# Kernel optimization log

Measured on AMD Instinct MI355X. Metric: run time of the kernel, lower is better.

## Reference

```python
import jax, jax.numpy as jnp
import numpy as np

NUM_CLASSES = 10
NPTS = 100            # quadrature points per unit interval (torch default npts=100)
EPS = 1e-5            # self.epsilon in the torch module
BATCH = 131072
C_IN = 512


def _betaln(a, b):
    return jax.lax.lgamma(a) + jax.lax.lgamma(b) - jax.lax.lgamma(a + b)


def setup_inputs() -> dict:
    key = jax.random.key(0)
    k1, k2, k3, k4, k5 = jax.random.split(key, 5)
    s = 1.0 / np.sqrt(C_IN).astype(np.float32)
    x = jax.random.normal(k1, (BATCH, C_IN), dtype=jnp.float32)
    W_alpha = jax.random.normal(k2, (C_IN, 1), dtype=jnp.float32) * s
    b_alpha = jax.random.normal(k3, (1,), dtype=jnp.float32) * s
    W_beta = jax.random.normal(k4, (C_IN, 1), dtype=jnp.float32) * s
    b_beta = jax.random.normal(k5, (1,), dtype=jnp.float32) * s
    return {"x": x, "W_alpha": W_alpha, "b_alpha": b_alpha,
            "W_beta": W_beta, "b_beta": b_beta}


def reference(x, W_alpha, b_alpha, W_beta, b_beta):
    # alpha, beta: [B, 1], clamp(1 + softplus(linear(x)), 1, 100)
    alpha = jnp.clip(1.0 + jax.nn.softplus(x @ W_alpha + b_alpha), 1.0, 100.0)
    beta = jnp.clip(1.0 + jax.nn.softplus(x @ W_beta + b_beta), 1.0, 100.0)
    lbeta = _betaln(alpha, beta)  # [B, 1] log Beta-function normalizer
    dx = 1.0 / (NPTS * NUM_CLASSES)

    def unnorm_cdf(b_thr):
        # torch: linspace(eps, b-eps, int(npts*b)); Beta.log_prob broadcast [B, n]
        n = int(NPTS * b_thr)
        if n == 0:
            return jnp.zeros((x.shape[0],), dtype=x.dtype)
        grid = jnp.linspace(EPS, b_thr - EPS, n, dtype=x.dtype)  # [n]
        logpdf = ((alpha - 1.0) * jnp.log(grid)
                  + (beta - 1.0) * jnp.log1p(-grid)
                  - lbeta)  # [B, n]
        return jnp.exp(logpdf).sum(axis=1) * dx  # [B]

    # thresholds i/C for i = 0..C (static Python loop over C+1 small fixed set)
    cdfs = [unnorm_cdf(i / NUM_CLASSES) for i in range(NUM_CLASSES + 1)]
    probs = jnp.stack([cdfs[i + 1] - cdfs[i] for i in range(NUM_CLASSES)], axis=1)  # [B, C]
    # torch uses diag(1/rowsum) @ probs == row-broadcast normalization
    return probs / probs.sum(axis=1, keepdims=True)
```

## Files before the change

kernel.cpp:

```cpp
#include <hip/hip_runtime.h>
#include <math.h>

#define EPS_F 1e-5f
#define NPOINTS 550
#define CIN 512

static __device__ __forceinline__ float softplus_f(float z) {
    return fmaxf(z, 0.0f) + log1pf(expf(-fabsf(z)));
}

static __device__ __forceinline__ float dot8(const float4 a0, const float4 a1,
                                             const float4 w0, const float4 w1) {
    float s = a0.x * w0.x;
    s = fmaf(a0.y, w0.y, s);
    s = fmaf(a0.z, w0.z, s);
    s = fmaf(a0.w, w0.w, s);
    s = fmaf(a1.x, w1.x, s);
    s = fmaf(a1.y, w1.y, s);
    s = fmaf(a1.z, w1.z, s);
    s = fmaf(a1.w, w1.w, s);
    return s;
}

__global__ __launch_bounds__(256, 8) void beta_unimodal_kernel(
    const float* __restrict__ x,
    const float* __restrict__ Wa, const float* __restrict__ ba,
    const float* __restrict__ Wb, const float* __restrict__ bb,
    float* __restrict__ out)
{
    __shared__ float2 tab[NPOINTS];
    __shared__ float outbuf[64 * 10];

    const int tid = threadIdx.x;

    for (int p = tid; p < NPOINTS; p += 256) {
        int i = 1, off = 0;
        while (p >= off + 10 * i) { off += 10 * i; ++i; }
        const int j = p - off;
        const int n = 10 * i;
        const float thr = (float)i * 0.1f;
        const float step = (thr - 2.0f * EPS_F) / (float)(n - 1);
        const float g = EPS_F + step * (float)j;
        float2 e;
        e.x = log2f(g);
        e.y = log2f(1.0f - g);
        tab[p] = e;
    }
    __syncthreads();

    const int lane = tid & 63;
    const int wave = tid >> 6;
    const long rowBase = (long)blockIdx.x * 64 + wave * 16;

    const float4* Wa4 = (const float4*)Wa;
    const float4* Wb4 = (const float4*)Wb;
    const float4 wa0 = Wa4[lane], wa1 = Wa4[64 + lane];
    const float4 wb0 = Wb4[lane], wb1 = Wb4[64 + lane];

    const int g = lane >> 2;
    const int q = lane & 3;
    float my_da = 0.0f, my_db = 0.0f;

    for (int r0 = 0; r0 < 16; r0 += 4) {
        float4 xs0[4], xs1[4];
        #pragma unroll
        for (int u = 0; u < 4; ++u) {
            const float4* xr = (const float4*)(x + (rowBase + r0 + u) * CIN);
            xs0[u] = xr[lane];
            xs1[u] = xr[64 + lane];
        }
        #pragma unroll
        for (int u = 0; u < 4; ++u) {
            float da = dot8(xs0[u], xs1[u], wa0, wa1);
            float db = dot8(xs0[u], xs1[u], wb0, wb1);
            #pragma unroll
            for (int s = 32; s > 0; s >>= 1) {
                da += __shfl_xor(da, s, 64);
                db += __shfl_xor(db, s, 64);
            }
            if (g == r0 + u) { my_da = da; my_db = db; }
        }
    }

    const float za = my_da + ba[0];
    const float zb = my_db + bb[0];
    const float alpha = fminf(fmaxf(1.0f + softplus_f(za), 1.0f), 100.0f);
    const float beta  = fminf(fmaxf(1.0f + softplus_f(zb), 1.0f), 100.0f);
    const float am1 = alpha - 1.0f;
    const float bm1 = beta - 1.0f;

    const float denom = am1 + bm1;
    float mode = (denom > 0.0f) ? (am1 / denom) : 0.5f;
    mode = fminf(fmaxf(mode, 1e-7f), 1.0f - 1.1920929e-7f);
    const float M2 = am1 * log2f(mode) + bm1 * log2f(1.0f - mode);

    float seg[10];
    int p0 = 0;
    #pragma unroll
    for (int i = 1; i <= 10; ++i) {
        const int n = 10 * i;
        float s = 0.0f;
        for (int j = q; j < n; j += 4) {
            const float2 t = tab[p0 + j];
            const float e = fmaf(am1, t.x, bm1 * t.y) - M2;
            s += __builtin_amdgcn_exp2f(e);
        }
        s += __shfl_xor(s, 1, 64);
        s += __shfl_xor(s, 2, 64);
        seg[i - 1] = s;
        p0 += n;
    }

    const float inv = 1.0f / seg[9];
    const int rowLocal = wave * 16 + g;
    for (int k = q; k < 10; k += 4) {
        const float prev = (k > 0) ? seg[k - 1] : 0.0f;
        outbuf[rowLocal * 10 + k] = (seg[k] - prev) * inv;
    }
    __syncthreads();

    if (tid < 160) {
        const float4* src = (const float4*)outbuf;
        float4* dst = (float4*)(out + (size_t)blockIdx.x * 640);
        dst[tid] = src[tid];
    }
}

extern "C" void kernel_launch(void* const* d_in, const int* in_sizes, int n_in,
                              void* d_out, int out_size, void* d_ws, size_t ws_size,
                              hipStream_t stream) {
    const float* x  = (const float*)d_in[0];
    const float* Wa = (const float*)d_in[1];
    const float* ba = (const float*)d_in[2];
    const float* Wb = (const float*)d_in[3];
    const float* bb = (const float*)d_in[4];
    float* out = (float*)d_out;

    const int batch = in_sizes[0] / CIN;
    const int blocks = batch / 64;
    beta_unimodal_kernel<<<blocks, 256, 0, stream>>>(x, Wa, ba, Wb, bb, out);
}
```

Measured before the change: 367.4 us.

## Replace per-row shuffle reductions with LDS transpose and halve rows per block

Each wave now computes partial dot products for 8 rows, writes them to shared memory, and reduces them with 8 lanes per row instead of 6-step full-wave shuffle reductions per row. Blocks cover 32 rows instead of 64, and the quadrature loop is split across 8 lanes per row rather than 4. The aim is to cut cross-lane shuffle cost and spread the exp work over more lanes. The extra ~17 KB of shared memory and the lower launch-bounds occupancy hint may limit the number of resident blocks.

```diff
diff --git a/kernel.cpp b/kernel.cpp
--- a/kernel.cpp
+++ b/kernel.cpp
@@ -22,14 +22,15 @@
     return s;
 }
 
-__global__ __launch_bounds__(256, 8) void beta_unimodal_kernel(
+__global__ __launch_bounds__(256, 4) void beta_unimodal_kernel(
     const float* __restrict__ x,
     const float* __restrict__ Wa, const float* __restrict__ ba,
     const float* __restrict__ Wb, const float* __restrict__ bb,
     float* __restrict__ out)
 {
     __shared__ float2 tab[NPOINTS];
-    __shared__ float outbuf[64 * 10];
+    __shared__ float outbuf[32 * 10];
+    __shared__ float part[4][2][8][68];
 
     const int tid = threadIdx.x;
 
@@ -50,37 +51,46 @@
 
     const int lane = tid & 63;
     const int wave = tid >> 6;
-    const long rowBase = (long)blockIdx.x * 64 + wave * 16;
+    const long rowBase = (long)blockIdx.x * 32 + wave * 8;
 
     const float4* Wa4 = (const float4*)Wa;
     const float4* Wb4 = (const float4*)Wb;
     const float4 wa0 = Wa4[lane], wa1 = Wa4[64 + lane];
     const float4 wb0 = Wb4[lane], wb1 = Wb4[64 + lane];
 
-    const int g = lane >> 2;
-    const int q = lane & 3;
-    float my_da = 0.0f, my_db = 0.0f;
+    float pa[8], pb[8];
+    #pragma unroll
+    for (int r = 0; r < 8; ++r) {
+        const float4* xr = (const float4*)(x + (rowBase + r) * CIN);
+        const float4 x0 = xr[lane];
+        const float4 x1 = xr[64 + lane];
+        pa[r] = dot8(x0, x1, wa0, wa1);
+        pb[r] = dot8(x0, x1, wb0, wb1);
+    }
 
-    for (int r0 = 0; r0 < 16; r0 += 4) {
-        float4 xs0[4], xs1[4];
-        #pragma unroll
-        for (int u = 0; u < 4; ++u) {
-            const float4* xr = (const float4*)(x + (rowBase + r0 + u) * CIN);
-            xs0[u] = xr[lane];
-            xs1[u] = xr[64 + lane];
-        }
-        #pragma unroll
-        for (int u = 0; u < 4; ++u) {
-            float da = dot8(xs0[u], xs1[u], wa0, wa1);
-            float db = dot8(xs0[u], xs1[u], wb0, wb1);
-            #pragma unroll
-            for (int s = 32; s > 0; s >>= 1) {
-                da += __shfl_xor(da, s, 64);
-                db += __shfl_xor(db, s, 64);
-            }
-            if (g == r0 + u) { my_da = da; my_db = db; }
-        }
+    #pragma unroll
+    for (int r = 0; r < 8; ++r) {
+        part[wave][0][r][lane] = pa[r];
+        part[wave][1][r][lane] = pb[r];
     }
+    asm volatile("s_waitcnt lgkmcnt(0)" ::: "memory");
+
+    const int row = lane >> 3;
+    const int o = lane & 7;
+    const int v = o >> 2;
+    const int qa = o & 3;
+    const float2* src2 = (const float2*)&part[wave][v][row][qa * 16];
+    float s = 0.0f;
+    #pragma unroll
+    for (int c = 0; c < 8; ++c) {
+        const float2 t = src2[c];
+        s += t.x + t.y;
+    }
+    s += __shfl_xor(s, 1, 64);
+    s += __shfl_xor(s, 2, 64);
+    const float other = __shfl_xor(s, 4, 64);
+    const float my_da = (v == 0) ? s : other;
+    const float my_db = (v == 0) ? other : s;
 
     const float za = my_da + ba[0];
     const float zb = my_db + bb[0];
@@ -99,29 +109,34 @@
     #pragma unroll
     for (int i = 1; i <= 10; ++i) {
         const int n = 10 * i;
-        float s = 0.0f;
-        for (int j = q; j < n; j += 4) {
+        float s2 = 0.0f;
+        for (int j = o; j < n; j += 8) {
             const float2 t = tab[p0 + j];
             const float e = fmaf(am1, t.x, bm1 * t.y) - M2;
-            s += __builtin_amdgcn_exp2f(e);
+            s2 += __builtin_amdgcn_exp2f(e);
         }
-        s += __shfl_xor(s, 1, 64);
-        s += __shfl_xor(s, 2, 64);
-        seg[i - 1] = s;
+        s2 += __shfl_xor(s2, 1, 64);
+        s2 += __shfl_xor(s2, 2, 64);
+        s2 += __shfl_xor(s2, 4, 64);
+        seg[i - 1] = s2;
         p0 += n;
     }
 
     const float inv = 1.0f / seg[9];
-    const int rowLocal = wave * 16 + g;
-    for (int k = q; k < 10; k += 4) {
-        const float prev = (k > 0) ? seg[k - 1] : 0.0f;
-        outbuf[rowLocal * 10 + k] = (seg[k] - prev) * inv;
+    const int rowLocal = wave * 8 + row;
+    {
+        const float prev = (o > 0) ? seg[o - 1] : 0.0f;
+        outbuf[rowLocal * 10 + o] = (seg[o] - prev) * inv;
+        if (o < 2) {
+            const int k = o + 8;
+            outbuf[rowLocal * 10 + k] = (seg[k] - seg[k - 1]) * inv;
+        }
     }
     __syncthreads();
 
-    if (tid < 160) {
+    if (tid < 80) {
         const float4* src = (const float4*)outbuf;
-        float4* dst = (float4*)(out + (size_t)blockIdx.x * 640);
+        float4* dst = (float4*)(out + (size_t)blockIdx.x * 320);
         dst[tid] = src[tid];
     }
 }
@@ -137,6 +152,6 @@
     float* out = (float*)d_out;
 
     const int batch = in_sizes[0] / CIN;
-    const int blocks = batch / 64;
+    const int blocks = batch / 32;
     beta_unimodal_kernel<<<blocks, 256, 0, stream>>>(x, Wa, ba, Wb, bb, out);
 }
```

Result: no change. 362.3 us (-1.4%).

## Split fused kernel into GEMV and per-thread quadrature kernels via workspace

Applied to the files above, without the earlier changes.

Splits the single fused kernel into two. The first is a GEMV kernel that double-buffers x row loads and reduces partial dot products through LDS plus shuffles, writing alpha/beta logits to the workspace. The second is a quadrature kernel in which each thread handles one full row, with no cross-lane shuffles, reading the table as float4 pairs. The split removes the serial coupling between the memory-bound dot products and the exp-heavy quadrature, at the cost of an extra launch and a workspace round trip.

```diff
diff --git a/kernel.cpp b/kernel.cpp
--- a/kernel.cpp
+++ b/kernel.cpp
@@ -22,14 +22,76 @@
     return s;
 }
 
-__global__ __launch_bounds__(256, 8) void beta_unimodal_kernel(
+__global__ __launch_bounds__(256, 4) void gemv_kernel(
     const float* __restrict__ x,
-    const float* __restrict__ Wa, const float* __restrict__ ba,
-    const float* __restrict__ Wb, const float* __restrict__ bb,
+    const float* __restrict__ Wa,
+    const float* __restrict__ Wb,
+    float* __restrict__ ws)
+{
+    __shared__ float part[4][4][68];
+
+    const int tid = threadIdx.x;
+    const int lane = tid & 63;
+    const int wave = tid >> 6;
+    const long waveRow0 = (long)blockIdx.x * 128 + wave * 32;
+
+    const float4* Wa4 = (const float4*)Wa;
+    const float4* Wb4 = (const float4*)Wb;
+    const float4 wa0 = Wa4[lane], wa1 = Wa4[64 + lane];
+    const float4 wb0 = Wb4[lane], wb1 = Wb4[64 + lane];
+
+    const int g = lane >> 4;
+    const int k = lane & 15;
+
+    float4 buf[2][4];
+    {
+        const float4* xr = (const float4*)(x + waveRow0 * CIN);
+        buf[0][0] = xr[lane];
+        buf[0][1] = xr[64 + lane];
+        buf[0][2] = xr[128 + lane];
+        buf[0][3] = xr[192 + lane];
+    }
+
+    #pragma unroll
+    for (int t = 0; t < 16; ++t) {
+        const int cur = t & 1;
+        if (t + 1 < 16) {
+            const float4* xn = (const float4*)(x + (waveRow0 + (t + 1) * 2) * CIN);
+            buf[cur ^ 1][0] = xn[lane];
+            buf[cur ^ 1][1] = xn[64 + lane];
+            buf[cur ^ 1][2] = xn[128 + lane];
+            buf[cur ^ 1][3] = xn[192 + lane];
+        }
+
+        const float pa0 = dot8(buf[cur][0], buf[cur][1], wa0, wa1);
+        const float pb0 = dot8(buf[cur][0], buf[cur][1], wb0, wb1);
+        const float pa1 = dot8(buf[cur][2], buf[cur][3], wa0, wa1);
+        const float pb1 = dot8(buf[cur][2], buf[cur][3], wb0, wb1);
+
+        part[wave][0][lane] = pa0;
+        part[wave][1][lane] = pb0;
+        part[wave][2][lane] = pa1;
+        part[wave][3][lane] = pb1;
+        asm volatile("s_waitcnt lgkmcnt(0)" ::: "memory");
+
+        const float4 q = *(const float4*)&part[wave][g][k * 4];
+        float s = (q.x + q.y) + (q.z + q.w);
+        s += __shfl_xor(s, 8, 64);
+        s += __shfl_xor(s, 4, 64);
+        s += __shfl_xor(s, 2, 64);
+        s += __shfl_xor(s, 1, 64);
+
+        if (k == 0) ws[(waveRow0 + t * 2) * 2 + g] = s;
+    }
+}
+
+__global__ __launch_bounds__(256, 4) void quad_kernel(
+    const float* __restrict__ ws,
+    const float* __restrict__ ba, const float* __restrict__ bb,
     float* __restrict__ out)
 {
-    __shared__ float2 tab[NPOINTS];
-    __shared__ float outbuf[64 * 10];
+    __shared__ __align__(16) float2 tab[NPOINTS];
+    __shared__ float outb[256 * 10];
 
     const int tid = threadIdx.x;
 
@@ -40,50 +102,18 @@
         const int n = 10 * i;
         const float thr = (float)i * 0.1f;
         const float step = (thr - 2.0f * EPS_F) / (float)(n - 1);
-        const float g = EPS_F + step * (float)j;
+        const float gx = EPS_F + step * (float)j;
         float2 e;
-        e.x = log2f(g);
-        e.y = log2f(1.0f - g);
+        e.x = log2f(gx);
+        e.y = log2f(1.0f - gx);
         tab[p] = e;
     }
     __syncthreads();
 
-    const int lane = tid & 63;
-    const int wave = tid >> 6;
-    const long rowBase = (long)blockIdx.x * 64 + wave * 16;
-
-    const float4* Wa4 = (const float4*)Wa;
-    const float4* Wb4 = (const float4*)Wb;
-    const float4 wa0 = Wa4[lane], wa1 = Wa4[64 + lane];
-    const float4 wb0 = Wb4[lane], wb1 = Wb4[64 + lane];
-
-    const int g = lane >> 2;
-    const int q = lane & 3;
-    float my_da = 0.0f, my_db = 0.0f;
-
-    for (int r0 = 0; r0 < 16; r0 += 4) {
-        float4 xs0[4], xs1[4];
-        #pragma unroll
-        for (int u = 0; u < 4; ++u) {
-            const float4* xr = (const float4*)(x + (rowBase + r0 + u) * CIN);
-            xs0[u] = xr[lane];
-            xs1[u] = xr[64 + lane];
-        }
-        #pragma unroll
-        for (int u = 0; u < 4; ++u) {
-            float da = dot8(xs0[u], xs1[u], wa0, wa1);
-            float db = dot8(xs0[u], xs1[u], wb0, wb1);
-            #pragma unroll
-            for (int s = 32; s > 0; s >>= 1) {
-                da += __shfl_xor(da, s, 64);
-                db += __shfl_xor(db, s, 64);
-            }
-            if (g == r0 + u) { my_da = da; my_db = db; }
-        }
-    }
-
-    const float za = my_da + ba[0];
-    const float zb = my_db + bb[0];
+    const long row = (long)blockIdx.x * 256 + tid;
+    const float2 d = ((const float2*)ws)[row];
+    const float za = d.x + ba[0];
+    const float zb = d.y + bb[0];
     const float alpha = fminf(fmaxf(1.0f + softplus_f(za), 1.0f), 100.0f);
     const float beta  = fminf(fmaxf(1.0f + softplus_f(zb), 1.0f), 100.0f);
     const float am1 = alpha - 1.0f;
@@ -92,38 +122,37 @@
     const float denom = am1 + bm1;
     float mode = (denom > 0.0f) ? (am1 / denom) : 0.5f;
     mode = fminf(fmaxf(mode, 1e-7f), 1.0f - 1.1920929e-7f);
-    const float M2 = am1 * log2f(mode) + bm1 * log2f(1.0f - mode);
+    const float nM2 = -(am1 * log2f(mode) + bm1 * log2f(1.0f - mode));
 
     float seg[10];
     int p0 = 0;
     #pragma unroll
     for (int i = 1; i <= 10; ++i) {
         const int n = 10 * i;
-        float s = 0.0f;
-        for (int j = q; j < n; j += 4) {
-            const float2 t = tab[p0 + j];
-            const float e = fmaf(am1, t.x, bm1 * t.y) - M2;
-            s += __builtin_amdgcn_exp2f(e);
+        float s2 = 0.0f;
+        for (int j = 0; j < n; j += 2) {
+            const float4 tq = *(const float4*)&tab[p0 + j];
+            const float e0 = fmaf(am1, tq.x, fmaf(bm1, tq.y, nM2));
+            const float e1 = fmaf(am1, tq.z, fmaf(bm1, tq.w, nM2));
+            s2 += __builtin_amdgcn_exp2f(e0) + __builtin_amdgcn_exp2f(e1);
         }
-        s += __shfl_xor(s, 1, 64);
-        s += __shfl_xor(s, 2, 64);
-        seg[i - 1] = s;
+        seg[i - 1] = s2;
         p0 += n;
     }
 
     const float inv = 1.0f / seg[9];
-    const int rowLocal = wave * 16 + g;
-    for (int k = q; k < 10; k += 4) {
-        const float prev = (k > 0) ? seg[k - 1] : 0.0f;
-        outbuf[rowLocal * 10 + k] = (seg[k] - prev) * inv;
+    float prev = 0.0f;
+    #pragma unroll
+    for (int kk = 0; kk < 10; ++kk) {
+        outb[tid * 10 + kk] = (seg[kk] - prev) * inv;
+        prev = seg[kk];
     }
     __syncthreads();
 
-    if (tid < 160) {
-        const float4* src = (const float4*)outbuf;
-        float4* dst = (float4*)(out + (size_t)blockIdx.x * 640);
-        dst[tid] = src[tid];
-    }
+    const float4* s4 = (const float4*)outb;
+    float4* dst = (float4*)(out + (size_t)blockIdx.x * 2560);
+    #pragma unroll
+    for (int idx = tid; idx < 640; idx += 256) dst[idx] = s4[idx];
 }
 
 extern "C" void kernel_launch(void* const* d_in, const int* in_sizes, int n_in,
@@ -135,8 +164,9 @@
     const float* Wb = (const float*)d_in[3];
     const float* bb = (const float*)d_in[4];
     float* out = (float*)d_out;
+    float* ws  = (float*)d_ws;
 
     const int batch = in_sizes[0] / CIN;
-    const int blocks = batch / 64;
-    beta_unimodal_kernel<<<blocks, 256, 0, stream>>>(x, Wa, ba, Wb, bb, out);
+    gemv_kernel<<<batch / 128, 256, 0, stream>>>(x, Wa, Wb, ws);
+    quad_kernel<<<batch / 256, 256, 0, stream>>>(ws, ba, bb, out);
 }
```

Result: slower. 421.5 us (+14.7%).
